# Kernel tuning notes

Measured on AMD Instinct MI355X. Metric: run time of the kernel, lower is better.

The kernel has to match this reference:

```python
import jax, jax.numpy as jnp
import numpy as np

EMBED = 512
KDIM = 512
VDIM = 512
HEADS = 8
DHEAD = EMBED // HEADS  # 64
SCALE = 1.0 / np.sqrt(DHEAD).astype(np.float32)


def setup_inputs() -> dict:
    key = jax.random.key(0)
    ks = jax.random.split(key, 11)
    B, Lq, Lk = 4, 2048, 2048
    s_in = 1.0 / np.sqrt(EMBED).astype(np.float32)
    return {
        "query": jax.random.normal(ks[0], (B, Lq, EMBED), jnp.float32),
        "key": jax.random.normal(ks[1], (B, Lk, KDIM), jnp.float32),
        "value": jax.random.normal(ks[2], (B, Lk, VDIM), jnp.float32),
        "wq": jax.random.normal(ks[3], (EMBED, KDIM), jnp.float32) * s_in,
        "bq": jnp.zeros((KDIM,), jnp.float32),
        "wk": jax.random.normal(ks[4], (KDIM, KDIM), jnp.float32) * s_in,
        "bk": jnp.zeros((KDIM,), jnp.float32),
        "wv": jax.random.normal(ks[5], (VDIM, VDIM), jnp.float32) * s_in,
        "bv": jnp.zeros((VDIM,), jnp.float32),
        "wo": jax.random.normal(ks[6], (VDIM, EMBED), jnp.float32) * s_in,
        "bo": jnp.zeros((EMBED,), jnp.float32),
    }


def _split_heads(x):
    b, l, _ = x.shape
    return x.reshape(b, l, HEADS, DHEAD).transpose(0, 2, 1, 3)  # b h l d


def reference(query, key, value, wq, bq, wk, bk, wv, bv, wo, bo):
    # Linear projections (weights stored [in, out])
    q = _split_heads(query @ wq + bq)   # b h Lq d
    k = _split_heads(key @ wk + bk)     # b h Lk d
    v = _split_heads(value @ wv + bv)   # b h Lk d
    scores = jnp.einsum('bhid,bhjd->bhij', q, k) * SCALE  # b h Lq Lk
    attn = jax.nn.softmax(scores, axis=-1)
    # dropout is identity in eval mode
    ctx = jnp.einsum('bhij,bhjd->bhid', attn, v)  # b h Lq d
    b, h, l, d = ctx.shape
    ctx = ctx.transpose(0, 2, 1, 3).reshape(b, l, h * d)  # b Lq vdim
    return ctx @ wo + bo
```

## Files before the change

### kernel.cpp

```cpp
#include <hip/hip_runtime.h>
#include <stdint.h>

typedef unsigned short u16;
typedef unsigned int u32;
typedef __attribute__((ext_vector_type(8))) short short8;
typedef __attribute__((ext_vector_type(4))) float f32x4;
typedef __attribute__((ext_vector_type(16))) float f32x16;

#define DEVI static __device__ __forceinline__

DEVI u16 f2bf(float f) {
  union { float f; u32 u; } v; v.f = f;
  u32 r = v.u + 0x7FFFu + ((v.u >> 16) & 1u);
  return (u16)(r >> 16);
}

DEVI u32 pack2bf(float lo, float hi) {
  return (u32)f2bf(lo) | ((u32)f2bf(hi) << 16);
}

DEVI u32 pack2bf_fast(float lo, float hi) {
  union { float f; u32 u; } a, b;
  a.f = lo; b.f = hi;
  return __builtin_amdgcn_perm(b.u + 0x8000u, a.u + 0x8000u, 0x07060302u);
}

DEVI void gload_lds16(const u16* g, u16* l) {
  __builtin_amdgcn_global_load_lds((const __attribute__((address_space(1))) void*)g,
                                   (__attribute__((address_space(3))) void*)l, 16, 0, 0);
}

DEVI int sw8(int chunk, int r) { return ((chunk ^ (r & 7) ^ ((r >> 3) & 3)) * 8); }

__global__ __launch_bounds__(256) void tw4(const float* __restrict__ s0, const float* __restrict__ s1,
                                           const float* __restrict__ s2, const float* __restrict__ s3,
                                           u16* __restrict__ d0, u16* __restrict__ d1,
                                           u16* __restrict__ d2, u16* __restrict__ d3) {
  int z = blockIdx.z;
  const float* src = z == 0 ? s0 : z == 1 ? s1 : z == 2 ? s2 : s3;
  u16* dst = z == 0 ? d0 : z == 1 ? d1 : z == 2 ? d2 : d3;
  __shared__ float tile[32][33];
  int tx = threadIdx.x & 31, ty = threadIdx.x >> 5;
  int bx = blockIdx.x * 32, by = blockIdx.y * 32;
#pragma unroll
  for (int i = 0; i < 32; i += 8)
    tile[ty + i][tx] = src[(size_t)(by + ty + i) * 512 + bx + tx];
  __syncthreads();
#pragma unroll
  for (int i = 0; i < 32; i += 8)
    dst[(size_t)(bx + ty + i) * 512 + by + tx] = f2bf(tile[tx][ty + i]);
}

__global__ __launch_bounds__(256) void gemm_qkv(
    const float* __restrict__ A0, const float* __restrict__ A1, const float* __restrict__ A2,
    const u16* __restrict__ W0, const u16* __restrict__ W1, const u16* __restrict__ W2,
    const float* __restrict__ b0, const float* __restrict__ b1, const float* __restrict__ b2,
    u16* __restrict__ oq, u16* __restrict__ ok, u16* __restrict__ vt, float qscale) {
  const int z = blockIdx.z;
  const float* A = z == 0 ? A0 : z == 1 ? A1 : A2;
  const u16* WT = z == 0 ? W0 : z == 1 ? W1 : W2;
  const float* bias = z == 0 ? b0 : z == 1 ? b1 : b2;
  const float sc = z == 0 ? qscale : 1.0f;

  __shared__ __align__(16) u16 As[128 * 64];
  __shared__ __align__(16) u16 Bs[128 * 64];
  const int t = threadIdx.x;
  const int w = t >> 6, lane = t & 63, quad = lane >> 4, li = lane & 15;
  const int m0 = blockIdx.x * 128, n0 = blockIdx.y * 128;
  const int wm = (w >> 1) * 64, wn = (w & 1) * 64;

  f32x4 zv = {0.f, 0.f, 0.f, 0.f};
  f32x4 acc[4][4];
#pragma unroll
  for (int mi = 0; mi < 4; mi++)
#pragma unroll
    for (int ni = 0; ni < 4; ni++) acc[mi][ni] = zv;

  const int rA = t >> 3, cA = t & 7;
  for (int it = 0; it < 8; it++) {
    const int k0 = it * 64;
#pragma unroll
    for (int p = 0; p < 4; p++) {
      int r = p * 32 + rA;
      const float* ga = A + (size_t)(m0 + r) * 512 + k0 + cA * 8;
      float4 f0 = *(const float4*)ga;
      float4 f1 = *(const float4*)(ga + 4);
      uint4 pk;
      pk.x = pack2bf_fast(f0.x, f0.y);
      pk.y = pack2bf_fast(f0.z, f0.w);
      pk.z = pack2bf_fast(f1.x, f1.y);
      pk.w = pack2bf_fast(f1.z, f1.w);
      *(uint4*)&As[r * 64 + sw8(cA, r)] = pk;
    }
#pragma unroll
    for (int p = 0; p < 4; p++) {
      int s = p * 256 + t;
      int r = s >> 3, c8 = s & 7;
      gload_lds16(WT + (size_t)(n0 + r) * 512 + k0 + sw8(c8, r), &Bs[(p * 256 + w * 64) * 8]);
    }
    __syncthreads();
#pragma unroll
    for (int ks = 0; ks < 2; ks++) {
      short8 af[4], bf[4];
#pragma unroll
      for (int mi = 0; mi < 4; mi++) {
        int r = wm + mi * 16 + li;
        af[mi] = *(const short8*)&As[r * 64 + sw8(ks * 4 + quad, r)];
      }
#pragma unroll
      for (int ni = 0; ni < 4; ni++) {
        int r = wn + ni * 16 + li;
        bf[ni] = *(const short8*)&Bs[r * 64 + sw8(ks * 4 + quad, r)];
      }
#pragma unroll
      for (int mi = 0; mi < 4; mi++)
#pragma unroll
        for (int ni = 0; ni < 4; ni++)
          acc[mi][ni] = __builtin_amdgcn_mfma_f32_16x16x32_bf16(af[mi], bf[ni], acc[mi][ni], 0, 0, 0);
    }
    __syncthreads();
  }

  float bv[4];
#pragma unroll
  for (int ni = 0; ni < 4; ni++) bv[ni] = bias[n0 + wn + ni * 16 + li];

  if (z < 2) {
    u16* out = z == 0 ? oq : ok;
#pragma unroll
    for (int mi = 0; mi < 4; mi++)
#pragma unroll
      for (int ni = 0; ni < 4; ni++)
#pragma unroll
        for (int r = 0; r < 4; r++) {
          int row = m0 + wm + mi * 16 + quad * 4 + r;
          int col = n0 + wn + ni * 16 + li;
          out[(size_t)row * 512 + col] = f2bf((acc[mi][ni][r] + bv[ni]) * sc);
        }
  } else {
#pragma unroll
    for (int mi = 0; mi < 4; mi++)
#pragma unroll
      for (int ni = 0; ni < 4; ni++) {
        int col = n0 + wn + ni * 16 + li;
        int h = col >> 6, dd = col & 63;
        int row0 = m0 + wm + mi * 16 + quad * 4;
        int bb = row0 >> 11, l0 = row0 & 2047;
        uint2 dw;
        dw.x = pack2bf(acc[mi][ni][0] + bv[ni], acc[mi][ni][1] + bv[ni]);
        dw.y = pack2bf(acc[mi][ni][2] + bv[ni], acc[mi][ni][3] + bv[ni]);
        *(uint2*)&vt[((size_t)((bb * 8 + h) * 64 + dd)) * 2048 + l0] = dw;
      }
  }
}

__global__ __launch_bounds__(256) void gemm_out(const u16* __restrict__ A,
                                                const u16* __restrict__ WT,
                                                const float* __restrict__ bias,
                                                float* __restrict__ out) {
  __shared__ __align__(16) u16 As[128 * 64];
  __shared__ __align__(16) u16 Bs[128 * 64];
  const int t = threadIdx.x;
  const int w = t >> 6, lane = t & 63, quad = lane >> 4, li = lane & 15;
  const int m0 = blockIdx.x * 128, n0 = blockIdx.y * 128;
  const int wm = (w >> 1) * 64, wn = (w & 1) * 64;

  f32x4 zv = {0.f, 0.f, 0.f, 0.f};
  f32x4 acc[4][4];
#pragma unroll
  for (int mi = 0; mi < 4; mi++)
#pragma unroll
    for (int ni = 0; ni < 4; ni++) acc[mi][ni] = zv;

  for (int it = 0; it < 8; it++) {
    const int k0 = it * 64;
#pragma unroll
    for (int p = 0; p < 4; p++) {
      int s = p * 256 + t;
      int r = s >> 3, c8 = s & 7;
      gload_lds16(A + (size_t)(m0 + r) * 512 + k0 + sw8(c8, r), &As[(p * 256 + w * 64) * 8]);
      gload_lds16(WT + (size_t)(n0 + r) * 512 + k0 + sw8(c8, r), &Bs[(p * 256 + w * 64) * 8]);
    }
    __syncthreads();
#pragma unroll
    for (int ks = 0; ks < 2; ks++) {
      short8 af[4], bf[4];
#pragma unroll
      for (int mi = 0; mi < 4; mi++) {
        int r = wm + mi * 16 + li;
        af[mi] = *(const short8*)&As[r * 64 + sw8(ks * 4 + quad, r)];
      }
#pragma unroll
      for (int ni = 0; ni < 4; ni++) {
        int r = wn + ni * 16 + li;
        bf[ni] = *(const short8*)&Bs[r * 64 + sw8(ks * 4 + quad, r)];
      }
#pragma unroll
      for (int mi = 0; mi < 4; mi++)
#pragma unroll
        for (int ni = 0; ni < 4; ni++)
          acc[mi][ni] = __builtin_amdgcn_mfma_f32_16x16x32_bf16(af[mi], bf[ni], acc[mi][ni], 0, 0, 0);
    }
    __syncthreads();
  }

  float bv[4];
#pragma unroll
  for (int ni = 0; ni < 4; ni++) bv[ni] = bias[n0 + wn + ni * 16 + li];
#pragma unroll
  for (int mi = 0; mi < 4; mi++)
#pragma unroll
    for (int ni = 0; ni < 4; ni++)
#pragma unroll
      for (int r = 0; r < 4; r++) {
        int row = m0 + wm + mi * 16 + quad * 4 + r;
        int col = n0 + wn + ni * 16 + li;
        out[(size_t)row * 512 + col] = acc[mi][ni][r] + bv[ni];
      }
}

__global__ __launch_bounds__(128) void attn(const u16* __restrict__ Qp,
                                            const u16* __restrict__ Kp,
                                            const u16* __restrict__ VT,
                                            float* __restrict__ Op,
                                            float* __restrict__ Lb) {
  __shared__ __align__(16) u16 Ks[64 * 64];
  __shared__ __align__(16) u16 Vs[64 * 64];
  __shared__ __align__(16) u16 Ps[4][32 * 64];
  const int t = threadIdx.x;
  const int w = t >> 6, lane = t & 63, qn = lane & 31, hi = lane >> 5;
  const int b = blockIdx.z, h = blockIdx.y >> 1, s = blockIdx.y & 1;
  const int q0 = blockIdx.x * 128;

  u16* Qs = &Ps[0][0];
#pragma unroll
  for (int i = 0; i < 8; i++) {
    int si = i * 128 + t;
    int r = si >> 3, c8 = si & 7;
    gload_lds16(Qp + (size_t)(b * 2048 + q0 + r) * 512 + h * 64 + sw8(c8, r),
                &Qs[(i * 128 + w * 64) * 8]);
  }
  __syncthreads();
  short8 qf[2][4];
#pragma unroll
  for (int u = 0; u < 2; u++)
#pragma unroll
    for (int ks = 0; ks < 4; ks++) {
      int rq = w * 64 + u * 32 + qn;
      qf[u][ks] = *(const short8*)&Qs[rq * 64 + sw8(ks * 2 + hi, rq)];
    }

  f32x16 o[2][2];
#pragma unroll
  for (int u = 0; u < 2; u++)
#pragma unroll
    for (int dt = 0; dt < 2; dt++)
#pragma unroll
      for (int r = 0; r < 16; r++) o[u][dt][r] = 0.f;
  float lsum[2] = {0.f, 0.f};

  for (int kt = s * 16; kt < s * 16 + 16; kt++) {
    const int k0 = kt * 64;
#pragma unroll
    for (int i = 0; i < 4; i++) {
      int si = i * 128 + t;
      int r = si >> 3, c8 = si & 7;
      gload_lds16(Kp + (size_t)(b * 2048 + k0 + r) * 512 + h * 64 + sw8(c8, r),
                  &Ks[(i * 128 + w * 64) * 8]);
      gload_lds16(VT + ((size_t)((b * 8 + h) * 64 + r)) * 2048 + k0 + sw8(c8, r),
                  &Vs[(i * 128 + w * 64) * 8]);
    }
    __syncthreads();

#pragma unroll
    for (int u = 0; u < 2; u++) {
      f32x16 st[2];
#pragma unroll
      for (int kjt = 0; kjt < 2; kjt++) {
#pragma unroll
        for (int r = 0; r < 16; r++) st[kjt][r] = 0.f;
#pragma unroll
        for (int ks = 0; ks < 4; ks++) {
          int m = kjt * 32 + qn;
          short8 ka = *(const short8*)&Ks[m * 64 + sw8(ks * 2 + hi, m)];
          st[kjt] = __builtin_amdgcn_mfma_f32_32x32x16_bf16(ka, qf[u][ks], st[kjt], 0, 0, 0);
        }
      }

      u16* pw = &Ps[w * 2 + u][0];
#pragma unroll
      for (int kjt = 0; kjt < 2; kjt++)
#pragma unroll
        for (int k8 = 0; k8 < 4; k8++) {
          float p0 = __builtin_amdgcn_exp2f(st[kjt][k8 * 4 + 0]);
          float p1 = __builtin_amdgcn_exp2f(st[kjt][k8 * 4 + 1]);
          float p2 = __builtin_amdgcn_exp2f(st[kjt][k8 * 4 + 2]);
          float p3 = __builtin_amdgcn_exp2f(st[kjt][k8 * 4 + 3]);
          lsum[u] += (p0 + p1) + (p2 + p3);
          uint2 dw;
          dw.x = pack2bf_fast(p0, p1);
          dw.y = pack2bf_fast(p2, p3);
          *(uint2*)&pw[qn * 64 + sw8(kjt * 4 + k8, qn) + hi * 4] = dw;
        }

      short8 pb[4];
#pragma unroll
      for (int ks = 0; ks < 4; ks++)
        pb[ks] = *(const short8*)&pw[qn * 64 + sw8(ks * 2 + hi, qn)];
#pragma unroll
      for (int dt = 0; dt < 2; dt++)
#pragma unroll
        for (int ks = 0; ks < 4; ks++) {
          int m = dt * 32 + qn;
          short8 va = *(const short8*)&Vs[m * 64 + sw8(ks * 2 + hi, m)];
          o[u][dt] = __builtin_amdgcn_mfma_f32_32x32x16_bf16(va, pb[ks], o[u][dt], 0, 0, 0);
        }
    }
    __syncthreads();
  }

#pragma unroll
  for (int u = 0; u < 2; u++) {
    float l = lsum[u] + __shfl_xor(lsum[u], 32);
    int qg = q0 + w * 64 + u * 32 + qn;
    if (hi == 0) Lb[((size_t)((b * 8 + h) * 2 + s)) * 2048 + qg] = l;
#pragma unroll
    for (int dt = 0; dt < 2; dt++)
#pragma unroll
      for (int r = 0; r < 16; r++) {
        int d = dt * 32 + (r & 3) + 8 * (r >> 2) + 4 * hi;
        Op[((size_t)(((b * 8 + h) * 2 + s) * 64 + d)) * 2048 + qg] = o[u][dt][r];
      }
  }
}

__global__ __launch_bounds__(256) void reduce_o(const float* __restrict__ Op,
                                                const float* __restrict__ Lb,
                                                u16* __restrict__ ctx) {
  __shared__ float tile[64 * 65];
  const int t = threadIdx.x;
  const int b = blockIdx.z, h = blockIdx.y, q0 = blockIdx.x * 64;
  {
    int d = t >> 2, qc = (t & 3) * 16;
    const float* p0 = Op + ((size_t)(((b * 8 + h) * 2 + 0) * 64 + d)) * 2048 + q0 + qc;
    const float* p1 = Op + ((size_t)(((b * 8 + h) * 2 + 1) * 64 + d)) * 2048 + q0 + qc;
#pragma unroll
    for (int i = 0; i < 4; i++) {
      float4 a = *(const float4*)(p0 + i * 4);
      float4 c = *(const float4*)(p1 + i * 4);
      float4 v;
      v.x = a.x + c.x; v.y = a.y + c.y; v.z = a.z + c.z; v.w = a.w + c.w;
      *(float4*)&tile[d * 65 + qc + i * 4] = v;
    }
  }
  __syncthreads();
  {
    int q = t >> 2, dc = (t & 3) * 16;
    float l0 = Lb[((size_t)((b * 8 + h) * 2 + 0)) * 2048 + q0 + q];
    float l1 = Lb[((size_t)((b * 8 + h) * 2 + 1)) * 2048 + q0 + q];
    float inv = 1.0f / (l0 + l1);
    u32 pk[8];
#pragma unroll
    for (int i = 0; i < 8; i++) {
      float v0 = tile[(dc + i * 2) * 65 + q] * inv;
      float v1 = tile[(dc + i * 2 + 1) * 65 + q] * inv;
      pk[i] = pack2bf(v0, v1);
    }
    u16* dst = ctx + (size_t)(b * 2048 + q0 + q) * 512 + h * 64 + dc;
    *(uint4*)dst = *(uint4*)&pk[0];
    *(uint4*)(dst + 8) = *(uint4*)&pk[4];
  }
}

extern "C" void kernel_launch(void* const* d_in, const int* in_sizes, int n_in,
                              void* d_out, int out_size, void* d_ws, size_t ws_size,
                              hipStream_t stream) {
  const float* query = (const float*)d_in[0];
  const float* key_ = (const float*)d_in[1];
  const float* value = (const float*)d_in[2];
  const float* wq = (const float*)d_in[3];
  const float* bq = (const float*)d_in[4];
  const float* wk = (const float*)d_in[5];
  const float* bk = (const float*)d_in[6];
  const float* wv = (const float*)d_in[7];
  const float* bv = (const float*)d_in[8];
  const float* wo = (const float*)d_in[9];
  const float* bo = (const float*)d_in[10];

  char* ws = (char*)d_ws;
  const size_t SZ_W = (size_t)512 * 512 * 2;
  const size_t SZ_X = (size_t)8192 * 512 * 2;
  u16* wqT = (u16*)(ws);
  u16* wkT = (u16*)(ws + SZ_W);
  u16* wvT = (u16*)(ws + 2 * SZ_W);
  u16* woT = (u16*)(ws + 3 * SZ_W);
  u16* Qp = (u16*)(ws + 4 * SZ_W);
  u16* Kp = (u16*)(ws + 4 * SZ_W + SZ_X);
  u16* VTp = (u16*)(ws + 4 * SZ_W + 2 * SZ_X);
  float* Opb = (float*)(ws + 4 * SZ_W + 3 * SZ_X);
  float* Lb = (float*)(ws + 4 * SZ_W + 3 * SZ_X + ((size_t)32 << 20));
  u16* ctx = Qp;

  const float C1 = 0.125f * 1.44269504088896f;

  tw4<<<dim3(16, 16, 4), 256, 0, stream>>>(wq, wk, wv, wo, wqT, wkT, wvT, woT);
  gemm_qkv<<<dim3(64, 4, 3), 256, 0, stream>>>(query, key_, value, wqT, wkT, wvT,
                                               bq, bk, bv, Qp, Kp, VTp, C1);
  attn<<<dim3(16, 16, 4), 128, 0, stream>>>(Qp, Kp, VTp, Opb, Lb);
  reduce_o<<<dim3(32, 8, 4), 256, 0, stream>>>(Opb, Lb, ctx);
  gemm_out<<<dim3(64, 4), 256, 0, stream>>>(ctx, woT, bo, (float*)d_out);
}
```

Measured before the change: 210.4 us.

## Use one query tile per wave in attention and halve gemm_out N tile

```diff
diff --git a/kernel.cpp b/kernel.cpp
--- a/kernel.cpp
+++ b/kernel.cpp
@@ -159,18 +159,18 @@
                                                 const float* __restrict__ bias,
                                                 float* __restrict__ out) {
   __shared__ __align__(16) u16 As[128 * 64];
-  __shared__ __align__(16) u16 Bs[128 * 64];
+  __shared__ __align__(16) u16 Bs[64 * 64];
   const int t = threadIdx.x;
   const int w = t >> 6, lane = t & 63, quad = lane >> 4, li = lane & 15;
-  const int m0 = blockIdx.x * 128, n0 = blockIdx.y * 128;
-  const int wm = (w >> 1) * 64, wn = (w & 1) * 64;
+  const int m0 = blockIdx.x * 128, n0 = blockIdx.y * 64;
+  const int wm = (w >> 1) * 64, wn = (w & 1) * 32;
 
   f32x4 zv = {0.f, 0.f, 0.f, 0.f};
-  f32x4 acc[4][4];
+  f32x4 acc[4][2];
 #pragma unroll
   for (int mi = 0; mi < 4; mi++)
 #pragma unroll
-    for (int ni = 0; ni < 4; ni++) acc[mi][ni] = zv;
+    for (int ni = 0; ni < 2; ni++) acc[mi][ni] = zv;
 
   for (int it = 0; it < 8; it++) {
     const int k0 = it * 64;
@@ -179,38 +179,43 @@
       int s = p * 256 + t;
       int r = s >> 3, c8 = s & 7;
       gload_lds16(A + (size_t)(m0 + r) * 512 + k0 + sw8(c8, r), &As[(p * 256 + w * 64) * 8]);
+    }
+#pragma unroll
+    for (int p = 0; p < 2; p++) {
+      int s = p * 256 + t;
+      int r = s >> 3, c8 = s & 7;
       gload_lds16(WT + (size_t)(n0 + r) * 512 + k0 + sw8(c8, r), &Bs[(p * 256 + w * 64) * 8]);
     }
     __syncthreads();
 #pragma unroll
     for (int ks = 0; ks < 2; ks++) {
-      short8 af[4], bf[4];
+      short8 af[4], bf[2];
 #pragma unroll
       for (int mi = 0; mi < 4; mi++) {
         int r = wm + mi * 16 + li;
         af[mi] = *(const short8*)&As[r * 64 + sw8(ks * 4 + quad, r)];
       }
 #pragma unroll
-      for (int ni = 0; ni < 4; ni++) {
+      for (int ni = 0; ni < 2; ni++) {
         int r = wn + ni * 16 + li;
         bf[ni] = *(const short8*)&Bs[r * 64 + sw8(ks * 4 + quad, r)];
       }
 #pragma unroll
       for (int mi = 0; mi < 4; mi++)
 #pragma unroll
-        for (int ni = 0; ni < 4; ni++)
+        for (int ni = 0; ni < 2; ni++)
           acc[mi][ni] = __builtin_amdgcn_mfma_f32_16x16x32_bf16(af[mi], bf[ni], acc[mi][ni], 0, 0, 0);
     }
     __syncthreads();
   }
 
-  float bv[4];
-#pragma unroll
-  for (int ni = 0; ni < 4; ni++) bv[ni] = bias[n0 + wn + ni * 16 + li];
+  float bv[2];
+#pragma unroll
+  for (int ni = 0; ni < 2; ni++) bv[ni] = bias[n0 + wn + ni * 16 + li];
 #pragma unroll
   for (int mi = 0; mi < 4; mi++)
 #pragma unroll
-    for (int ni = 0; ni < 4; ni++)
+    for (int ni = 0; ni < 2; ni++)
 #pragma unroll
       for (int r = 0; r < 4; r++) {
         int row = m0 + wm + mi * 16 + quad * 4 + r;
@@ -219,11 +224,11 @@
       }
 }
 
-__global__ __launch_bounds__(128) void attn(const u16* __restrict__ Qp,
-                                            const u16* __restrict__ Kp,
-                                            const u16* __restrict__ VT,
-                                            float* __restrict__ Op,
-                                            float* __restrict__ Lb) {
+__global__ __launch_bounds__(256, 4) void attn(const u16* __restrict__ Qp,
+                                               const u16* __restrict__ Kp,
+                                               const u16* __restrict__ VT,
+                                               float* __restrict__ Op,
+                                               float* __restrict__ Lb) {
   __shared__ __align__(16) u16 Ks[64 * 64];
   __shared__ __align__(16) u16 Vs[64 * 64];
   __shared__ __align__(16) u16 Ps[4][32 * 64];
@@ -231,107 +236,89 @@
   const int w = t >> 6, lane = t & 63, qn = lane & 31, hi = lane >> 5;
   const int b = blockIdx.z, h = blockIdx.y >> 1, s = blockIdx.y & 1;
   const int q0 = blockIdx.x * 128;
-
-  u16* Qs = &Ps[0][0];
-#pragma unroll
-  for (int i = 0; i < 8; i++) {
-    int si = i * 128 + t;
-    int r = si >> 3, c8 = si & 7;
-    gload_lds16(Qp + (size_t)(b * 2048 + q0 + r) * 512 + h * 64 + sw8(c8, r),
-                &Qs[(i * 128 + w * 64) * 8]);
-  }
-  __syncthreads();
-  short8 qf[2][4];
-#pragma unroll
-  for (int u = 0; u < 2; u++)
-#pragma unroll
-    for (int ks = 0; ks < 4; ks++) {
-      int rq = w * 64 + u * 32 + qn;
-      qf[u][ks] = *(const short8*)&Qs[rq * 64 + sw8(ks * 2 + hi, rq)];
-    }
-
-  f32x16 o[2][2];
-#pragma unroll
-  for (int u = 0; u < 2; u++)
-#pragma unroll
-    for (int dt = 0; dt < 2; dt++)
-#pragma unroll
-      for (int r = 0; r < 16; r++) o[u][dt][r] = 0.f;
-  float lsum[2] = {0.f, 0.f};
+  const int qrow = q0 + w * 32 + qn;
+
+  short8 qf[4];
+  {
+    const u16* qg = Qp + (size_t)(b * 2048 + qrow) * 512 + h * 64 + hi * 8;
+#pragma unroll
+    for (int ks = 0; ks < 4; ks++) qf[ks] = *(const short8*)(qg + ks * 16);
+  }
+
+  f32x16 o[2];
+#pragma unroll
+  for (int dt = 0; dt < 2; dt++)
+#pragma unroll
+    for (int r = 0; r < 16; r++) o[dt][r] = 0.f;
+  float lsum = 0.f;
+
+  u16* pw = &Ps[w][0];
 
   for (int kt = s * 16; kt < s * 16 + 16; kt++) {
     const int k0 = kt * 64;
 #pragma unroll
-    for (int i = 0; i < 4; i++) {
-      int si = i * 128 + t;
+    for (int i = 0; i < 2; i++) {
+      int si = i * 256 + t;
       int r = si >> 3, c8 = si & 7;
       gload_lds16(Kp + (size_t)(b * 2048 + k0 + r) * 512 + h * 64 + sw8(c8, r),
-                  &Ks[(i * 128 + w * 64) * 8]);
+                  &Ks[(i * 256 + w * 64) * 8]);
       gload_lds16(VT + ((size_t)((b * 8 + h) * 64 + r)) * 2048 + k0 + sw8(c8, r),
-                  &Vs[(i * 128 + w * 64) * 8]);
-    }
-    __syncthreads();
-
-#pragma unroll
-    for (int u = 0; u < 2; u++) {
-      f32x16 st[2];
-#pragma unroll
-      for (int kjt = 0; kjt < 2; kjt++) {
-#pragma unroll
-        for (int r = 0; r < 16; r++) st[kjt][r] = 0.f;
-#pragma unroll
-        for (int ks = 0; ks < 4; ks++) {
-          int m = kjt * 32 + qn;
-          short8 ka = *(const short8*)&Ks[m * 64 + sw8(ks * 2 + hi, m)];
-          st[kjt] = __builtin_amdgcn_mfma_f32_32x32x16_bf16(ka, qf[u][ks], st[kjt], 0, 0, 0);
-        }
-      }
-
-      u16* pw = &Ps[w * 2 + u][0];
-#pragma unroll
-      for (int kjt = 0; kjt < 2; kjt++)
-#pragma unroll
-        for (int k8 = 0; k8 < 4; k8++) {
-          float p0 = __builtin_amdgcn_exp2f(st[kjt][k8 * 4 + 0]);
-          float p1 = __builtin_amdgcn_exp2f(st[kjt][k8 * 4 + 1]);
-          float p2 = __builtin_amdgcn_exp2f(st[kjt][k8 * 4 + 2]);
-          float p3 = __builtin_amdgcn_exp2f(st[kjt][k8 * 4 + 3]);
-          lsum[u] += (p0 + p1) + (p2 + p3);
-          uint2 dw;
-          dw.x = pack2bf_fast(p0, p1);
-          dw.y = pack2bf_fast(p2, p3);
-          *(uint2*)&pw[qn * 64 + sw8(kjt * 4 + k8, qn) + hi * 4] = dw;
-        }
-
-      short8 pb[4];
-#pragma unroll
-      for (int ks = 0; ks < 4; ks++)
-        pb[ks] = *(const short8*)&pw[qn * 64 + sw8(ks * 2 + hi, qn)];
-#pragma unroll
-      for (int dt = 0; dt < 2; dt++)
-#pragma unroll
-        for (int ks = 0; ks < 4; ks++) {
-          int m = dt * 32 + qn;
-          short8 va = *(const short8*)&Vs[m * 64 + sw8(ks * 2 + hi, m)];
-          o[u][dt] = __builtin_amdgcn_mfma_f32_32x32x16_bf16(va, pb[ks], o[u][dt], 0, 0, 0);
-        }
-    }
-    __syncthreads();
-  }
-
-#pragma unroll
-  for (int u = 0; u < 2; u++) {
-    float l = lsum[u] + __shfl_xor(lsum[u], 32);
-    int qg = q0 + w * 64 + u * 32 + qn;
-    if (hi == 0) Lb[((size_t)((b * 8 + h) * 2 + s)) * 2048 + qg] = l;
+                  &Vs[(i * 256 + w * 64) * 8]);
+    }
+    __syncthreads();
+
+    f32x16 st[2];
+#pragma unroll
+    for (int kjt = 0; kjt < 2; kjt++) {
+#pragma unroll
+      for (int r = 0; r < 16; r++) st[kjt][r] = 0.f;
+#pragma unroll
+      for (int ks = 0; ks < 4; ks++) {
+        int m = kjt * 32 + qn;
+        short8 ka = *(const short8*)&Ks[m * 64 + sw8(ks * 2 + hi, m)];
+        st[kjt] = __builtin_amdgcn_mfma_f32_32x32x16_bf16(ka, qf[ks], st[kjt], 0, 0, 0);
+      }
+    }
+
+#pragma unroll
+    for (int kjt = 0; kjt < 2; kjt++)
+#pragma unroll
+      for (int k8 = 0; k8 < 4; k8++) {
+        float p0 = __builtin_amdgcn_exp2f(st[kjt][k8 * 4 + 0]);
+        float p1 = __builtin_amdgcn_exp2f(st[kjt][k8 * 4 + 1]);
+        float p2 = __builtin_amdgcn_exp2f(st[kjt][k8 * 4 + 2]);
+        float p3 = __builtin_amdgcn_exp2f(st[kjt][k8 * 4 + 3]);
+        lsum += (p0 + p1) + (p2 + p3);
+        uint2 dw;
+        dw.x = pack2bf_fast(p0, p1);
+        dw.y = pack2bf_fast(p2, p3);
+        *(uint2*)&pw[qn * 64 + sw8(kjt * 4 + k8, qn) + hi * 4] = dw;
+      }
+
+    short8 pb[4];
+#pragma unroll
+    for (int ks = 0; ks < 4; ks++)
+      pb[ks] = *(const short8*)&pw[qn * 64 + sw8(ks * 2 + hi, qn)];
 #pragma unroll
     for (int dt = 0; dt < 2; dt++)
 #pragma unroll
-      for (int r = 0; r < 16; r++) {
-        int d = dt * 32 + (r & 3) + 8 * (r >> 2) + 4 * hi;
-        Op[((size_t)(((b * 8 + h) * 2 + s) * 64 + d)) * 2048 + qg] = o[u][dt][r];
-      }
-  }
+      for (int ks = 0; ks < 4; ks++) {
+        int m = dt * 32 + qn;
+        short8 va = *(const short8*)&Vs[m * 64 + sw8(ks * 2 + hi, m)];
+        o[dt] = __builtin_amdgcn_mfma_f32_32x32x16_bf16(va, pb[ks], o[dt], 0, 0, 0);
+      }
+    __syncthreads();
+  }
+
+  float l = lsum + __shfl_xor(lsum, 32);
+  if (hi == 0) Lb[((size_t)((b * 8 + h) * 2 + s)) * 2048 + qrow] = l;
+#pragma unroll
+  for (int dt = 0; dt < 2; dt++)
+#pragma unroll
+    for (int r = 0; r < 16; r++) {
+      int d = dt * 32 + (r & 3) + 8 * (r >> 2) + 4 * hi;
+      Op[((size_t)(((b * 8 + h) * 2 + s) * 64 + d)) * 2048 + qrow] = o[dt][r];
+    }
 }
 
 __global__ __launch_bounds__(256) void reduce_o(const float* __restrict__ Op,
@@ -406,7 +393,7 @@
   tw4<<<dim3(16, 16, 4), 256, 0, stream>>>(wq, wk, wv, wo, wqT, wkT, wvT, woT);
   gemm_qkv<<<dim3(64, 4, 3), 256, 0, stream>>>(query, key_, value, wqT, wkT, wvT,
                                                bq, bk, bv, Qp, Kp, VTp, C1);
-  attn<<<dim3(16, 16, 4), 128, 0, stream>>>(Qp, Kp, VTp, Opb, Lb);
+  attn<<<dim3(16, 16, 4), 256, 0, stream>>>(Qp, Kp, VTp, Opb, Lb);
   reduce_o<<<dim3(32, 8, 4), 256, 0, stream>>>(Opb, Lb, ctx);
-  gemm_out<<<dim3(64, 4), 256, 0, stream>>>(ctx, woT, bo, (float*)d_out);
-}
+  gemm_out<<<dim3(64, 8), 256, 0, stream>>>(ctx, woT, bo, (float*)d_out);
+}
```

Measured after the change: 199.3 us. 5.2% less time.
